# Optimization experiments

Hardware: AMD Instinct MI355X
Metric: run time of the kernel (lower is better)

Reference implementation:

```python
import jax, jax.numpy as jnp
import numpy as np

N = 16384      # number of points
DIM = 128      # feature dim
POS_DIM = 3
K = 16         # neighbors (init kwarg k)
SCALE = np.float32(np.sqrt(DIM))


def setup_inputs() -> dict:
    key = jax.random.key(0)
    ks = jax.random.split(key, 16)
    g = lambda i, shape: (jax.random.normal(ks[i], shape, dtype=jnp.float32) * 0.05)
    return {
        "x": jax.random.normal(ks[0], (N, DIM), dtype=jnp.float32),
        "pos": jax.random.uniform(ks[1], (N, POS_DIM), dtype=jnp.float32),
        # weights stored as (in, out); torch Linear applies x @ W.T + b
        "Wq": g(2, (DIM, DIM)),
        "Wk": g(3, (DIM, DIM)),
        "Wv": g(4, (DIM, DIM)),
        "mid_w1": g(5, (DIM, DIM)), "mid_b1": g(6, (DIM,)),
        "mid_w2": g(7, (DIM, DIM)), "mid_b2": g(8, (DIM,)),
        "pe_w1": g(9, (POS_DIM, DIM)), "pe_b1": g(10, (DIM,)),
        "pe_w2": g(11, (DIM, DIM)), "pe_b2": g(12, (DIM,)),
        "fin_w": g(13, (DIM, DIM)), "fin_b": g(14, (DIM,)),
    }


def _knn_indices(pos):
    # squared pairwise distances [N, N]; top-K smallest -> neighbor indices [N, K]
    sq = jnp.sum(pos * pos, axis=-1)
    d2 = sq[:, None] + sq[None, :] - 2.0 * (pos @ pos.T)
    _, ind = jax.lax.top_k(-d2, K)
    return ind


def reference(x, pos, Wq, Wk, Wv, mid_w1, mid_b1, mid_w2, mid_b2,
              pe_w1, pe_b1, pe_w2, pe_b2, fin_w, fin_b):
    ind = _knn_indices(pos)                    # [N, K] int32 (constant wrt grads)
    x_k = x[ind]                               # [N, K, D]
    pos_k = pos[ind]                           # [N, K, 3]
    rel = pos[:, None, :] - pos_k              # [N, K, 3]
    pe = jax.nn.relu(rel @ pe_w1 + pe_b1) @ pe_w2 + pe_b2    # [N, K, D]
    q = x @ Wq                                 # [N, D]
    h = q[:, None, :] - (x_k @ Wk) + pe        # [N, K, D]
    y = jax.nn.relu(h @ mid_w1 + mid_b1) @ mid_w2 + mid_b2   # [N, K, D]
    y = jax.nn.softmax(y / SCALE, axis=-2)     # softmax over neighbors K
    z = x_k @ Wv + pe                          # [N, K, D]
    agg = jnp.sum(y * z, axis=-2)              # [N, D]
    return agg @ fin_w + fin_b + x
```

## Files before the change

kernel.cpp:

```cpp
#include <hip/hip_runtime.h>
#include <hip/hip_bf16.h>

#define N_PTS 16384
#define DIMF  128
#define KNB   16
#define GRES  8
#define NCELL (GRES*GRES*GRES)

typedef __attribute__((ext_vector_type(8))) short bf16x8;
typedef __attribute__((ext_vector_type(4))) short bf16x4;
typedef __attribute__((ext_vector_type(4))) float f32x4;
typedef __attribute__((ext_vector_type(4))) unsigned int u32x4;
typedef __attribute__((ext_vector_type(2))) unsigned int u32x2;

__device__ __forceinline__ unsigned short f2b(float f){
  unsigned int u = __float_as_uint(f);
  u = u + 0x7fffu + ((u >> 16) & 1u);
  return (unsigned short)(u >> 16);
}
__device__ __forceinline__ unsigned cvtpk(float lo, float hi){
  unsigned r;
  asm("v_cvt_pk_bf16_f32 %0, %1, %2" : "=v"(r) : "v"(lo), "v"(hi));
  return r;
}
__device__ __forceinline__ float b2f(unsigned short u){
  return __uint_as_float(((unsigned)u) << 16);
}
__device__ __forceinline__ float b2fs(short s){
  return __uint_as_float(((unsigned)(unsigned short)s) << 16);
}
__device__ __forceinline__ float unsort_f(unsigned s){
  unsigned u = (s & 0x80000000u) ? (s ^ 0x80000000u) : ~s;
  return __uint_as_float(u);
}

__global__ __launch_bounds__(256) void count_kernel(const float* __restrict__ pos, int* __restrict__ cnt){
  int i = blockIdx.x*256 + threadIdx.x;
  float px = pos[i*3+0], py = pos[i*3+1], pz = pos[i*3+2];
  int cx = min(GRES-1, max(0,(int)(px*(float)GRES)));
  int cy = min(GRES-1, max(0,(int)(py*(float)GRES)));
  int cz = min(GRES-1, max(0,(int)(pz*(float)GRES)));
  atomicAdd(&cnt[(cz*GRES+cy)*GRES+cx], 1);
}

__global__ __launch_bounds__(256) void scan_kernel(const int* __restrict__ cnt, int* __restrict__ starts, int* __restrict__ fillp){
  __shared__ int part[256];
  int t = threadIdx.x;
  int a = cnt[2*t], b = cnt[2*t+1];
  part[t] = a + b;
  __syncthreads();
  if (t == 0){
    int acc = 0;
    for (int i=0;i<256;++i){ int tmp = part[i]; part[i] = acc; acc += tmp; }
  }
  __syncthreads();
  int base = part[t];
  starts[2*t]   = base;     fillp[2*t]   = base;
  starts[2*t+1] = base + a; fillp[2*t+1] = base + a;
}

__global__ __launch_bounds__(256) void scatter_kernel(const float* __restrict__ pos, int* __restrict__ fillp,
                                                      float4* __restrict__ pos4, int* __restrict__ pidx,
                                                      int* __restrict__ inv){
  int i = blockIdx.x*256 + threadIdx.x;
  float px = pos[i*3+0], py = pos[i*3+1], pz = pos[i*3+2];
  int cx = min(GRES-1, max(0,(int)(px*(float)GRES)));
  int cy = min(GRES-1, max(0,(int)(py*(float)GRES)));
  int cz = min(GRES-1, max(0,(int)(pz*(float)GRES)));
  int c = (cz*GRES+cy)*GRES+cx;
  float sq = __fadd_rn(__fadd_rn(__fmul_rn(px,px), __fmul_rn(py,py)), __fmul_rn(pz,pz));
  int s = atomicAdd(&fillp[c], 1);
  pos4[s] = make_float4(px, py, pz, sq);
  pidx[s] = i;
  inv[i] = s;
}

__global__ __launch_bounds__(256) void knn_query64(const float4* __restrict__ pos4, const int* __restrict__ pidx,
                                                   const int* __restrict__ starts, const int* __restrict__ cnt,
                                                   const int* __restrict__ inv,
                                                   int* __restrict__ ind_slot, char* __restrict__ flags){
  __shared__ unsigned long long cand[4][64];
  int lane = threadIdx.x & 63;
  int wv   = threadIdx.x >> 6;
  int t = blockIdx.x*4 + wv;
  float4 qp = pos4[t];
  float qx = qp.x, qy = qp.y, qz = qp.z, qsq = qp.w;
  int cx = min(GRES-1, max(0,(int)(qx*(float)GRES)));
  int cy = min(GRES-1, max(0,(int)(qy*(float)GRES)));
  int cz = min(GRES-1, max(0,(int)(qz*(float)GRES)));
  int zlo = max(0,cz-1), zhi = min(GRES-1,cz+1);
  int ylo = max(0,cy-1), yhi = min(GRES-1,cy+1);
  int xlo = max(0,cx-1), xhi = min(GRES-1,cx+1);

  int nb = 0;
  if (lane < 27){
    int dz = lane/9 - 1, dy = (lane/3)%3 - 1, dx = lane%3 - 1;
    int zz = cz+dz, yy = cy+dy, xx = cx+dx;
    if (zz>=zlo && zz<=zhi && yy>=ylo && yy<=yhi && xx>=xlo && xx<=xhi)
      nb = cnt[(zz*GRES+yy)*GRES+xx];
  }
  #pragma unroll
  for (int o=1;o<64;o<<=1) nb += __shfl_xor(nb, o, 64);
  float V = (float)((zhi-zlo+1)*(yhi-ylo+1)*(xhi-xlo+1)) * 0.001953125f;
  float r3 = 3.8197186f * V / (float)nb;
  float tau2 = 2.0f * __powf(r3, 0.66666667f);

  int nfound = 0;
  bool okscan = false;
  for (int it = 0; it < 8; ++it){
    nfound = 0;
    for (int zz=zlo; zz<=zhi; ++zz)
    for (int yy=ylo; yy<=yhi; ++yy)
    for (int xx=xlo; xx<=xhi; ++xx){
      int c = (zz*GRES+yy)*GRES+xx;
      int s0 = starts[c], n = cnt[c];
      for (int b = 0; b < n; b += 64){
        int o = b + lane;
        bool valid = o < n;
        float d = 3.0e38f; int idx = 0;
        if (valid){
          float4 pc = pos4[s0+o];
          idx = pidx[s0+o];
          float dot = __fmaf_rn(qz, pc.z, __fmaf_rn(qy, pc.y, __fmul_rn(qx, pc.x)));
          d   = __fsub_rn(__fadd_rn(qsq, pc.w), __fmul_rn(2.0f, dot));
        }
        bool admit = valid && (d < tau2);
        unsigned long long mask = __ballot(admit);
        if (admit){
          int pos = nfound + (int)__popcll(mask & ((1ull<<lane)-1ull));
          if (pos < 64){
            unsigned su = __float_as_uint(d);
            su ^= (unsigned)((int)su >> 31) | 0x80000000u;
            cand[wv][pos] = ((unsigned long long)su << 32) | (unsigned)idx;
          }
        }
        nfound += (int)__popcll(mask);
      }
    }
    if (nfound > 64){ tau2 *= 0.7f; continue; }
    if (nfound < 16){ tau2 *= 2.0f; continue; }
    okscan = true; break;
  }
  if (!okscan){ if (lane == 0) flags[t] = 1; return; }

  asm volatile("s_waitcnt lgkmcnt(0)" ::: "memory");
  __builtin_amdgcn_sched_barrier(0);
  unsigned long long key = (lane < nfound) ? cand[wv][lane] : ~0ull;

  #pragma unroll
  for (int k = 2; k <= 64; k <<= 1){
    #pragma unroll
    for (int j = k>>1; j >= 1; j >>= 1){
      unsigned long long other = __shfl_xor(key, j, 64);
      bool takeSmall = (((lane & k) == 0) != ((lane & j) != 0));
      bool less = other < key;
      key = (takeSmall == less) ? other : key;
    }
  }
  if (lane < 16) ind_slot[t*KNB + lane] = inv[(int)(unsigned)(key & 0xffffffffu)];

  unsigned long long k15 = __shfl(key, 15, 64);
  float b16 = unsort_f((unsigned)(k15 >> 32));
  double mg = 1.0e300;
  double dqx=(double)qx, dqy=(double)qy, dqz=(double)qz;
  const double h = 0.125;
  if (cx-1 > 0)      mg = fmin(mg, dqx - (double)(cx-1)*h);
  if (cx+1 < GRES-1) mg = fmin(mg, (double)(cx+2)*h - dqx);
  if (cy-1 > 0)      mg = fmin(mg, dqy - (double)(cy-1)*h);
  if (cy+1 < GRES-1) mg = fmin(mg, (double)(cy+2)*h - dqy);
  if (cz-1 > 0)      mg = fmin(mg, dqz - (double)(cz-1)*h);
  if (cz+1 < GRES-1) mg = fmin(mg, (double)(cz+2)*h - dqz);
  bool ok = (mg*mg > (double)b16 + 1.0e-5);
  if (lane == 0) flags[t] = ok ? 0 : 1;
}

__global__ __launch_bounds__(256) void knn_fallback(const float4* __restrict__ pos4, const int* __restrict__ pidx,
                                                    const int* __restrict__ starts, const int* __restrict__ cnt,
                                                    const int* __restrict__ inv,
                                                    const char* __restrict__ flags, int* __restrict__ ind_slot){
  int t = blockIdx.x*256 + threadIdx.x;
  if (t >= N_PTS || !flags[t]) return;
  float4 qp = pos4[t];
  float qx = qp.x, qy = qp.y, qz = qp.z, qsq = qp.w;
  int cx = min(GRES-1, max(0,(int)(qx*(float)GRES)));
  int cy = min(GRES-1, max(0,(int)(qy*(float)GRES)));
  int cz = min(GRES-1, max(0,(int)(qz*(float)GRES)));
  float bd[KNB]; int bi[KNB];
  #pragma unroll
  for (int k=0;k<KNB;++k){ bd[k] = 3.0e38f; bi[k] = 0x7fffffff; }
  const double cinv = 0.125;
  for (int r = 0; r < GRES; ++r){
    int zlo = max(0, cz-r), zhi = min(GRES-1, cz+r);
    int ylo = max(0, cy-r), yhi = min(GRES-1, cy+r);
    int xlo = max(0, cx-r), xhi = min(GRES-1, cx+r);
    for (int zz = zlo; zz <= zhi; ++zz){
      for (int yy = ylo; yy <= yhi; ++yy){
        for (int xx = xlo; xx <= xhi; ++xx){
          int ring = max(abs(zz-cz), max(abs(yy-cy), abs(xx-cx)));
          if (ring != r) continue;
          int c = (zz*GRES+yy)*GRES+xx;
          int s0 = starts[c], e = s0 + cnt[c];
          for (int s = s0; s < e; ++s){
            float4 pc = pos4[s];
            int idx = pidx[s];
            float dot = __fmaf_rn(qz, pc.z, __fmaf_rn(qy, pc.y, __fmul_rn(qx, pc.x)));
            float d   = __fsub_rn(__fadd_rn(qsq, pc.w), __fmul_rn(2.0f, dot));
            bool adm = (d < bd[KNB-1]) || (d == bd[KNB-1] && idx < bi[KNB-1]);
            if (adm){
              #pragma unroll
              for (int p = KNB-1; p >= 1; --p){
                float pd = bd[p-1]; int pi = bi[p-1];
                bool sh  = (pd > d) || (pd == d && pi > idx);
                bool ins = (!sh) && ((bd[p] > d) || (bd[p] == d && bi[p] > idx));
                bd[p] = sh ? pd : (ins ? d   : bd[p]);
                bi[p] = sh ? pi : (ins ? idx : bi[p]);
              }
              bool s0b = (bd[0] > d) || (bd[0] == d && bi[0] > idx);
              if (s0b){ bd[0] = d; bi[0] = idx; }
            }
          }
        }
      }
    }
    if (bd[KNB-1] < 3.0e37f){
      double mg = 1.0e300;
      double dqx=(double)qx, dqy=(double)qy, dqz=(double)qz;
      if (cx - r > 0)      mg = fmin(mg, dqx - (double)(cx-r)*cinv);
      if (cx + r < GRES-1) mg = fmin(mg, (double)(cx+r+1)*cinv - dqx);
      if (cy - r > 0)      mg = fmin(mg, dqy - (double)(cy-r)*cinv);
      if (cy + r < GRES-1) mg = fmin(mg, (double)(cy+r+1)*cinv - dqy);
      if (cz - r > 0)      mg = fmin(mg, dqz - (double)(cz-r)*cinv);
      if (cz + r < GRES-1) mg = fmin(mg, (double)(cz+r+1)*cinv - dqz);
      if (mg*mg > (double)bd[KNB-1] + 1.0e-5) break;
    }
  }
  #pragma unroll
  for (int k=0;k<KNB;++k) ind_slot[t*KNB + k] = inv[bi[k]];
}

__global__ __launch_bounds__(256) void pack_all(const float* __restrict__ w0, const float* __restrict__ w1,
                                                const float* __restrict__ w2, const float* __restrict__ w3,
                                                const float* __restrict__ w4, const float* __restrict__ w5,
                                                const float* __restrict__ w6,
                                                short* __restrict__ dst){
  int slot = blockIdx.y;
  const float* src = (slot==0)?w0:(slot==1)?w1:(slot==2)?w2:(slot==3)?w3:(slot==4)?w4:(slot==5)?w5:w6;
  int f = blockIdx.x*256 + threadIdx.x;
  int j  = f & 7;
  int ln = (f >> 3) & 63;
  int ks = (f >> 9) & 3;
  int nt = f >> 11;
  int k = ks*32 + ((ln >> 4) << 3) + j;
  int n = nt*16 + (ln & 15);
  dst[slot*16384 + f] = (short)f2b(src[k*DIMF + n]);
}

__global__ __launch_bounds__(256) void proj_kernel(const float* __restrict__ x, const int* __restrict__ pidx,
                                                   const short* __restrict__ pw,
                                                   unsigned short* __restrict__ q, unsigned short* __restrict__ xk,
                                                   unsigned short* __restrict__ xv){
  __shared__ __align__(16) char Abuf[32768];
  int tid = threadIdx.x, lane = tid & 63, wv = tid >> 6;
  int r0 = blockIdx.x * 128;
  {
    int row = tid >> 1, half = tid & 1;
    int orig = pidx[r0 + row];
    const float4* xr = (const float4*)(x + (size_t)orig*DIMF + half*64);
    #pragma unroll
    for (int i=0;i<8;++i){
      float4 a = xr[2*i], b = xr[2*i+1];
      u32x4 u;
      u[0] = cvtpk(a.x, a.y); u[1] = cvtpk(a.z, a.w);
      u[2] = cvtpk(b.x, b.y); u[3] = cvtpk(b.z, b.w);
      *(u32x4*)(&Abuf[row*256 + ((half*128 + i*16) ^ ((row&7)<<4))]) = u;
    }
  }
  __syncthreads();
  #pragma unroll 1
  for (int w = 0; w < 3; ++w){
    const bf16x8* bw = (const bf16x8*)(pw + w*16384);
    unsigned short* dst = (w==0) ? q : (w==1) ? xk : xv;
    f32x4 acc[2][8];
    #pragma unroll
    for (int i=0;i<2;++i)
      #pragma unroll
      for (int nt=0;nt<8;++nt) acc[i][nt] = (f32x4){0.f,0.f,0.f,0.f};
    #pragma unroll
    for (int ks=0;ks<4;++ks){
      int ra = (wv*2)*16 + (lane&15);
      int rb = (wv*2+1)*16 + (lane&15);
      int cb = ks*64 + ((lane>>4)<<4);
      bf16x8 a0 = *(const bf16x8*)(&Abuf[ra*256 + (cb ^ ((ra&7)<<4))]);
      bf16x8 a1 = *(const bf16x8*)(&Abuf[rb*256 + (cb ^ ((rb&7)<<4))]);
      #pragma unroll
      for (int nt=0;nt<8;++nt){
        bf16x8 b = bw[(nt*4+ks)*64 + lane];
        acc[0][nt] = __builtin_amdgcn_mfma_f32_16x16x32_bf16(a0, b, acc[0][nt], 0, 0, 0);
        acc[1][nt] = __builtin_amdgcn_mfma_f32_16x16x32_bf16(a1, b, acc[1][nt], 0, 0, 0);
      }
    }
    #pragma unroll
    for (int i=0;i<2;++i){
      int mt = wv*2+i;
      #pragma unroll
      for (int nt=0;nt<8;++nt){
        int grow = r0 + mt*16 + ((lane>>4)<<2);
        int col = nt*16 + (lane&15);
        unsigned pk01 = cvtpk(acc[i][nt][0], acc[i][nt][1]);
        unsigned pk23 = cvtpk(acc[i][nt][2], acc[i][nt][3]);
        dst[(size_t)(grow+0)*DIMF + col] = (unsigned short)pk01;
        dst[(size_t)(grow+1)*DIMF + col] = (unsigned short)(pk01 >> 16);
        dst[(size_t)(grow+2)*DIMF + col] = (unsigned short)pk23;
        dst[(size_t)(grow+3)*DIMF + col] = (unsigned short)(pk23 >> 16);
      }
    }
  }
}

__global__ __launch_bounds__(512, 2) void main_kernel(
    const float* __restrict__ x, const float4* __restrict__ pos4, const int* __restrict__ pidx,
    const float* __restrict__ pe_w1, const float* __restrict__ pe_b1, const float* __restrict__ pe_b2,
    const float* __restrict__ mid_b1, const float* __restrict__ mid_b2, const float* __restrict__ fin_b,
    const unsigned short* __restrict__ qarr, const unsigned short* __restrict__ xkarr,
    const unsigned short* __restrict__ xvarr,
    const int* __restrict__ ind_slot, const short* __restrict__ pw,
    float* __restrict__ out)
{
  __shared__ __align__(16) char peLDS[32768];
  __shared__ __align__(16) char wbuf[32768];
  __shared__ float aggT[DIMF][8];
  __shared__ int indbuf[128];
  __shared__ int origbuf[8];
  int tid = threadIdx.x;
  int lane = tid & 63;
  int wv = tid >> 6;
  int t0 = blockIdx.x * 8;

  int g = lane >> 4, kl = lane & 15;
  int mt = wv;

  #define STAGE_W(slot) { \
    const char* gsrc = (const char*)(pw + (size_t)(slot)*16384) + wv*4096 + lane*16; \
    char* ldst = &wbuf[wv*4096]; \
    __builtin_amdgcn_global_load_lds(gsrc,        ldst,        16, 0, 0); \
    __builtin_amdgcn_global_load_lds(gsrc + 1024, ldst + 1024, 16, 0, 0); \
    __builtin_amdgcn_global_load_lds(gsrc + 2048, ldst + 2048, 16, 0, 0); \
    __builtin_amdgcn_global_load_lds(gsrc + 3072, ldst + 3072, 16, 0, 0); }

  if (tid < 128) indbuf[tid] = ind_slot[blockIdx.x*128 + tid];
  if (tid < 8) origbuf[tid] = pidx[t0 + tid];
  STAGE_W(3);
  __syncthreads();

  int nb4[4];
  #pragma unroll
  for (int r=0;r<4;++r) nb4[r] = indbuf[mt*16 + g*4 + r];
  int nbr = indbuf[mt*16 + kl];
  unsigned short zraw[8][4];
  #pragma unroll
  for (int nt=0;nt<8;++nt)
    #pragma unroll
    for (int r=0;r<4;++r)
      zraw[nt][r] = xvarr[(size_t)nb4[r]*DIMF + nt*16 + kl];

  bf16x8 tfrag[4];
  {
    float4 pq = pos4[t0+mt];
    float4 pn = pos4[nbr];
    float rx = pq.x-pn.x, ry = pq.y-pn.y, rz = pq.z-pn.z;
    #pragma unroll
    for (int ks=0;ks<4;++ks){
      int c0 = ks*32 + g*8;
      const float4* w0 = (const float4*)(pe_w1 + c0);
      const float4* w1 = (const float4*)(pe_w1 + DIMF + c0);
      const float4* w2 = (const float4*)(pe_w1 + 2*DIMF + c0);
      const float4* bb = (const float4*)(pe_b1 + c0);
      float4 wa0=w0[0], wa1=w0[1], wb0=w1[0], wb1=w1[1], wc0=w2[0], wc1=w2[1], wd0=bb[0], wd1=bb[1];
      float wa[8]={wa0.x,wa0.y,wa0.z,wa0.w,wa1.x,wa1.y,wa1.z,wa1.w};
      float wb[8]={wb0.x,wb0.y,wb0.z,wb0.w,wb1.x,wb1.y,wb1.z,wb1.w};
      float wc[8]={wc0.x,wc0.y,wc0.z,wc0.w,wc1.x,wc1.y,wc1.z,wc1.w};
      float wd[8]={wd0.x,wd0.y,wd0.z,wd0.w,wd1.x,wd1.y,wd1.z,wd1.w};
      float tv[8];
      #pragma unroll
      for (int j=0;j<8;++j)
        tv[j] = fmaxf(fmaf(rx, wa[j], fmaf(ry, wb[j], fmaf(rz, wc[j], wd[j]))), 0.f);
      u32x4 u;
      u[0] = cvtpk(tv[0], tv[1]); u[1] = cvtpk(tv[2], tv[3]);
      u[2] = cvtpk(tv[4], tv[5]); u[3] = cvtpk(tv[6], tv[7]);
      tfrag[ks] = __builtin_bit_cast(bf16x8, u);
    }
  }

  f32x4 acc[8];
  const bf16x8* bw = (const bf16x8*)wbuf;

  {
    #pragma unroll
    for (int nt=0;nt<8;++nt){
      float bv = pe_b2[nt*16 + kl];
      acc[nt] = (f32x4){bv,bv,bv,bv};
    }
    #pragma unroll
    for (int ks=0;ks<4;++ks){
      #pragma unroll
      for (int nt=0;nt<8;++nt){
        bf16x8 b = bw[(nt*4+ks)*64 + lane];
        acc[nt] = __builtin_amdgcn_mfma_f32_16x16x32_bf16(tfrag[ks], b, acc[nt], 0, 0, 0);
      }
    }
  }

  bf16x4 zb[8];
  int r0w = mt*16 + g*4;
  #pragma unroll
  for (int nt=0;nt<8;++nt){
    int col = nt*16 + kl;
    float p0 = acc[nt][0], p1 = acc[nt][1], p2 = acc[nt][2], p3 = acc[nt][3];
    unsigned pk01 = cvtpk(p0, p1), pk23 = cvtpk(p2, p3);
    *(unsigned short*)&peLDS[(r0w+0)*256 + ((col*2) ^ (((r0w+0)&7)<<4))] = (unsigned short)pk01;
    *(unsigned short*)&peLDS[(r0w+1)*256 + ((col*2) ^ (((r0w+1)&7)<<4))] = (unsigned short)(pk01 >> 16);
    *(unsigned short*)&peLDS[(r0w+2)*256 + ((col*2) ^ (((r0w+2)&7)<<4))] = (unsigned short)pk23;
    *(unsigned short*)&peLDS[(r0w+3)*256 + ((col*2) ^ (((r0w+3)&7)<<4))] = (unsigned short)(pk23 >> 16);
    float z0 = b2f(zraw[nt][0]) + p0;
    float z1 = b2f(zraw[nt][1]) + p1;
    float z2 = b2f(zraw[nt][2]) + p2;
    float z3 = b2f(zraw[nt][3]) + p3;
    u32x2 zu; zu[0] = cvtpk(z0, z1); zu[1] = cvtpk(z2, z3);
    zb[nt] = __builtin_bit_cast(bf16x4, zu);
  }

  bf16x8 q8[4], k8[4];
  {
    const unsigned short* qrow = qarr + (size_t)(t0+mt)*DIMF;
    const unsigned short* krow = xkarr + (size_t)nbr*DIMF;
    #pragma unroll
    for (int ks=0;ks<4;++ks){
      int c0 = ks*32 + g*8;
      q8[ks] = *(const bf16x8*)(qrow + c0);
      k8[ks] = *(const bf16x8*)(krow + c0);
    }
  }
  __syncthreads();
  STAGE_W(4);

  bf16x8 hfrag[4];
  {
    int row = mt*16 + kl;
    #pragma unroll
    for (int ks=0;ks<4;++ks){
      int c0 = ks*32 + g*8;
      bf16x8 p8 = *(const bf16x8*)(&peLDS[row*256 + ((c0*2) ^ ((row&7)<<4))]);
      float hf[8];
      #pragma unroll
      for (int j=0;j<8;++j)
        hf[j] = (b2fs(q8[ks][j]) - b2fs(k8[ks][j])) + b2fs(p8[j]);
      u32x4 u;
      u[0] = cvtpk(hf[0], hf[1]); u[1] = cvtpk(hf[2], hf[3]);
      u[2] = cvtpk(hf[4], hf[5]); u[3] = cvtpk(hf[6], hf[7]);
      hfrag[ks] = __builtin_bit_cast(bf16x8, u);
    }
  }
  __syncthreads();

  {
    #pragma unroll
    for (int nt=0;nt<8;++nt){
      float bv = mid_b1[nt*16 + kl];
      acc[nt] = (f32x4){bv,bv,bv,bv};
    }
    #pragma unroll
    for (int ks=0;ks<4;++ks){
      #pragma unroll
      for (int nt=0;nt<8;++nt){
        bf16x8 b = bw[(nt*4+ks)*64 + lane];
        acc[nt] = __builtin_amdgcn_mfma_f32_16x16x32_bf16(hfrag[ks], b, acc[nt], 0, 0, 0);
      }
    }
  }
  __syncthreads();
  STAGE_W(5);
  #pragma unroll
  for (int nt=0;nt<8;++nt){
    int col = nt*16 + kl;
    unsigned pk01 = cvtpk(fmaxf(acc[nt][0],0.f), fmaxf(acc[nt][1],0.f));
    unsigned pk23 = cvtpk(fmaxf(acc[nt][2],0.f), fmaxf(acc[nt][3],0.f));
    *(unsigned short*)&peLDS[(r0w+0)*256 + ((col*2) ^ (((r0w+0)&7)<<4))] = (unsigned short)pk01;
    *(unsigned short*)&peLDS[(r0w+1)*256 + ((col*2) ^ (((r0w+1)&7)<<4))] = (unsigned short)(pk01 >> 16);
    *(unsigned short*)&peLDS[(r0w+2)*256 + ((col*2) ^ (((r0w+2)&7)<<4))] = (unsigned short)pk23;
    *(unsigned short*)&peLDS[(r0w+3)*256 + ((col*2) ^ (((r0w+3)&7)<<4))] = (unsigned short)(pk23 >> 16);
  }
  __syncthreads();

  {
    #pragma unroll
    for (int nt=0;nt<8;++nt){
      float bv = mid_b2[nt*16 + kl];
      acc[nt] = (f32x4){bv,bv,bv,bv};
    }
    #pragma unroll
    for (int ks=0;ks<4;++ks){
      int ra = mt*16 + kl;
      int cb = ks*64 + g*16;
      bf16x8 a0 = *(const bf16x8*)(&peLDS[ra*256 + (cb ^ ((ra&7)<<4))]);
      #pragma unroll
      for (int nt=0;nt<8;++nt){
        bf16x8 b = bw[(nt*4+ks)*64 + lane];
        acc[nt] = __builtin_amdgcn_mfma_f32_16x16x32_bf16(a0, b, acc[nt], 0, 0, 0);
      }
    }
    const float invS = 0.08838834764831843f;
    #pragma unroll
    for (int nt=0;nt<8;++nt){
      f32x4 y = acc[nt];
      float mx = fmaxf(fmaxf(y[0],y[1]), fmaxf(y[2],y[3]));
      mx = fmaxf(mx, __shfl_xor(mx, 16, 64));
      mx = fmaxf(mx, __shfl_xor(mx, 32, 64));
      float e0 = __expf((y[0]-mx)*invS);
      float e1 = __expf((y[1]-mx)*invS);
      float e2 = __expf((y[2]-mx)*invS);
      float e3 = __expf((y[3]-mx)*invS);
      float ssum = e0+e1+e2+e3;
      ssum += __shfl_xor(ssum, 16, 64);
      ssum += __shfl_xor(ssum, 32, 64);
      bf16x4 zv = zb[nt];
      float ps = (e0*b2fs(zv[0]) + e1*b2fs(zv[1]) + e2*b2fs(zv[2]) + e3*b2fs(zv[3])) / ssum;
      ps += __shfl_xor(ps, 16, 64);
      ps += __shfl_xor(ps, 32, 64);
      if (lane < 16) aggT[nt*16 + lane][mt] = ps;
    }
  }
  __syncthreads();
  STAGE_W(6);
  __syncthreads();

  {
    f32x4 facc = (f32x4){0.f,0.f,0.f,0.f};
    #pragma unroll
    for (int ks=0;ks<4;++ks){
      int c0 = ks*32 + g*8;
      float av[8];
      #pragma unroll
      for (int j=0;j<8;++j)
        av[j] = (kl < 8) ? aggT[c0+j][kl] : 0.f;
      u32x4 u;
      u[0] = cvtpk(av[0], av[1]); u[1] = cvtpk(av[2], av[3]);
      u[2] = cvtpk(av[4], av[5]); u[3] = cvtpk(av[6], av[7]);
      bf16x8 a = __builtin_bit_cast(bf16x8, u);
      bf16x8 b = bw[(wv*4+ks)*64 + lane];
      facc = __builtin_amdgcn_mfma_f32_16x16x32_bf16(a, b, facc, 0, 0, 0);
    }
    int col = wv*16 + kl;
    float fb = fin_b[col];
    if (g < 2){
      #pragma unroll
      for (int r=0;r<4;++r){
        int prow = g*4 + r;
        int o = origbuf[prow];
        out[(size_t)o*DIMF + col] = facc[r] + fb + x[(size_t)o*DIMF + col];
      }
    }
  }
  #undef STAGE_W
}

extern "C" void kernel_launch(void* const* d_in, const int* in_sizes, int n_in,
                              void* d_out, int out_size, void* d_ws, size_t ws_size,
                              hipStream_t stream)
{
  (void)in_sizes; (void)n_in; (void)out_size; (void)ws_size;
  const float* x      = (const float*)d_in[0];
  const float* pos    = (const float*)d_in[1];
  const float* Wq     = (const float*)d_in[2];
  const float* Wk     = (const float*)d_in[3];
  const float* Wv     = (const float*)d_in[4];
  const float* mid_w1 = (const float*)d_in[5];
  const float* mid_b1 = (const float*)d_in[6];
  const float* mid_w2 = (const float*)d_in[7];
  const float* mid_b2 = (const float*)d_in[8];
  const float* pe_w1  = (const float*)d_in[9];
  const float* pe_b1  = (const float*)d_in[10];
  const float* pe_w2  = (const float*)d_in[11];
  const float* pe_b2  = (const float*)d_in[12];
  const float* fin_w  = (const float*)d_in[13];
  const float* fin_b  = (const float*)d_in[14];
  float* out = (float*)d_out;
  char* ws = (char*)d_ws;

  int*    cellcnt = (int*)   (ws + 0);
  int*    fillp   = (int*)   (ws + 4096);
  int*    starts  = (int*)   (ws + 8192);
  char*   flags   = (char*)  (ws + 18432);
  int*    pidx    = (int*)   (ws + 49152);
  float4* pos4    = (float4*)(ws + 114688);
  int*    ind     = (int*)   (ws + 376832);
  short*  pw      = (short*) (ws + 1425408);
  int*    inv     = (int*)   (ws + 1654784);
  unsigned short* qarr  = (unsigned short*)(ws + 1720320);
  unsigned short* xkarr = (unsigned short*)(ws + 5914624);
  unsigned short* xvarr = (unsigned short*)(ws + 10108928);

  hipMemsetAsync(cellcnt, 0, NCELL*sizeof(int), stream);
  count_kernel  <<<N_PTS/256, 256, 0, stream>>>(pos, cellcnt);
  scan_kernel   <<<1,         256, 0, stream>>>(cellcnt, starts, fillp);
  scatter_kernel<<<N_PTS/256, 256, 0, stream>>>(pos, fillp, pos4, pidx, inv);
  knn_query64   <<<N_PTS/4,   256, 0, stream>>>(pos4, pidx, starts, cellcnt, inv, ind, flags);
  knn_fallback  <<<N_PTS/256, 256, 0, stream>>>(pos4, pidx, starts, cellcnt, inv, flags, ind);

  pack_all<<<dim3(64,7), 256, 0, stream>>>(Wq, Wk, Wv, pe_w2, mid_w1, mid_w2, fin_w, pw);

  proj_kernel<<<N_PTS/128, 256, 0, stream>>>(x, pidx, pw, qarr, xkarr, xvarr);

  main_kernel<<<N_PTS/8, 512, 0, stream>>>(x, pos4, pidx, pe_w1, pe_b1, pe_b2, mid_b1, mid_b2, fin_b,
                                           qarr, xkarr, xvarr, ind, pw, out);
}
```

Measured before the change: 180.2 us.

## Parallelize cell scan, halve proj tile rows, pad aggT, overlap fin weight staging

Replaces the serial single-thread prefix sum in scan_kernel with a wave shuffle scan plus a cross-wave combine. proj_kernel now processes 64 rows per block instead of 128, which doubles the grid for more parallelism at the cost of reloading weights more often. aggT gets a padding column to reduce LDS bank conflicts. The fin_w staging load is moved before the softmax/aggregation epilogue so it overlaps that compute.

```diff
diff --git a/kernel.cpp b/kernel.cpp
--- a/kernel.cpp
+++ b/kernel.cpp
@@ -44,19 +44,24 @@
 }
 
 __global__ __launch_bounds__(256) void scan_kernel(const int* __restrict__ cnt, int* __restrict__ starts, int* __restrict__ fillp){
-  __shared__ int part[256];
+  __shared__ int wsum[4];
   int t = threadIdx.x;
+  int lane = t & 63, w = t >> 6;
   int a = cnt[2*t], b = cnt[2*t+1];
-  part[t] = a + b;
-  __syncthreads();
-  if (t == 0){
-    int acc = 0;
-    for (int i=0;i<256;++i){ int tmp = part[i]; part[i] = acc; acc += tmp; }
-  }
-  __syncthreads();
-  int base = part[t];
-  starts[2*t]   = base;     fillp[2*t]   = base;
-  starts[2*t+1] = base + a; fillp[2*t+1] = base + a;
+  int s = a + b;
+  int p = s;
+  #pragma unroll
+  for (int off = 1; off < 64; off <<= 1){
+    int v = __shfl_up(p, off, 64);
+    if (lane >= off) p += v;
+  }
+  if (lane == 63) wsum[w] = p;
+  __syncthreads();
+  int base = 0;
+  for (int i = 0; i < w; ++i) base += wsum[i];
+  int excl = base + p - s;
+  starts[2*t]   = excl;     fillp[2*t]   = excl;
+  starts[2*t+1] = excl + a; fillp[2*t+1] = excl + a;
 }
 
 __global__ __launch_bounds__(256) void scatter_kernel(const float* __restrict__ pos, int* __restrict__ fillp,
@@ -259,20 +264,20 @@
                                                    const short* __restrict__ pw,
                                                    unsigned short* __restrict__ q, unsigned short* __restrict__ xk,
                                                    unsigned short* __restrict__ xv){
-  __shared__ __align__(16) char Abuf[32768];
+  __shared__ __align__(16) char Abuf[16384];
   int tid = threadIdx.x, lane = tid & 63, wv = tid >> 6;
-  int r0 = blockIdx.x * 128;
-  {
-    int row = tid >> 1, half = tid & 1;
+  int r0 = blockIdx.x * 64;
+  {
+    int row = tid >> 2, q4 = tid & 3;
     int orig = pidx[r0 + row];
-    const float4* xr = (const float4*)(x + (size_t)orig*DIMF + half*64);
-    #pragma unroll
-    for (int i=0;i<8;++i){
+    const float4* xr = (const float4*)(x + (size_t)orig*DIMF + q4*32);
+    #pragma unroll
+    for (int i=0;i<4;++i){
       float4 a = xr[2*i], b = xr[2*i+1];
       u32x4 u;
       u[0] = cvtpk(a.x, a.y); u[1] = cvtpk(a.z, a.w);
       u[2] = cvtpk(b.x, b.y); u[3] = cvtpk(b.z, b.w);
-      *(u32x4*)(&Abuf[row*256 + ((half*128 + i*16) ^ ((row&7)<<4))]) = u;
+      *(u32x4*)(&Abuf[row*256 + ((q4*64 + i*16) ^ ((row&7)<<4))]) = u;
     }
   }
   __syncthreads();
@@ -280,39 +285,30 @@
   for (int w = 0; w < 3; ++w){
     const bf16x8* bw = (const bf16x8*)(pw + w*16384);
     unsigned short* dst = (w==0) ? q : (w==1) ? xk : xv;
-    f32x4 acc[2][8];
-    #pragma unroll
-    for (int i=0;i<2;++i)
-      #pragma unroll
-      for (int nt=0;nt<8;++nt) acc[i][nt] = (f32x4){0.f,0.f,0.f,0.f};
-    #pragma unroll
-    for (int ks=0;ks<4;++ks){
-      int ra = (wv*2)*16 + (lane&15);
-      int rb = (wv*2+1)*16 + (lane&15);
+    f32x4 acc[8];
+    #pragma unroll
+    for (int nt=0;nt<8;++nt) acc[nt] = (f32x4){0.f,0.f,0.f,0.f};
+    #pragma unroll
+    for (int ks=0;ks<4;++ks){
+      int ra = wv*16 + (lane&15);
       int cb = ks*64 + ((lane>>4)<<4);
       bf16x8 a0 = *(const bf16x8*)(&Abuf[ra*256 + (cb ^ ((ra&7)<<4))]);
-      bf16x8 a1 = *(const bf16x8*)(&Abuf[rb*256 + (cb ^ ((rb&7)<<4))]);
       #pragma unroll
       for (int nt=0;nt<8;++nt){
         bf16x8 b = bw[(nt*4+ks)*64 + lane];
-        acc[0][nt] = __builtin_amdgcn_mfma_f32_16x16x32_bf16(a0, b, acc[0][nt], 0, 0, 0);
-        acc[1][nt] = __builtin_amdgcn_mfma_f32_16x16x32_bf16(a1, b, acc[1][nt], 0, 0, 0);
+        acc[nt] = __builtin_amdgcn_mfma_f32_16x16x32_bf16(a0, b, acc[nt], 0, 0, 0);
       }
     }
     #pragma unroll
-    for (int i=0;i<2;++i){
-      int mt = wv*2+i;
-      #pragma unroll
-      for (int nt=0;nt<8;++nt){
-        int grow = r0 + mt*16 + ((lane>>4)<<2);
-        int col = nt*16 + (lane&15);
-        unsigned pk01 = cvtpk(acc[i][nt][0], acc[i][nt][1]);
-        unsigned pk23 = cvtpk(acc[i][nt][2], acc[i][nt][3]);
-        dst[(size_t)(grow+0)*DIMF + col] = (unsigned short)pk01;
-        dst[(size_t)(grow+1)*DIMF + col] = (unsigned short)(pk01 >> 16);
-        dst[(size_t)(grow+2)*DIMF + col] = (unsigned short)pk23;
-        dst[(size_t)(grow+3)*DIMF + col] = (unsigned short)(pk23 >> 16);
-      }
+    for (int nt=0;nt<8;++nt){
+      int grow = r0 + wv*16 + ((lane>>4)<<2);
+      int col = nt*16 + (lane&15);
+      unsigned pk01 = cvtpk(acc[nt][0], acc[nt][1]);
+      unsigned pk23 = cvtpk(acc[nt][2], acc[nt][3]);
+      dst[(size_t)(grow+0)*DIMF + col] = (unsigned short)pk01;
+      dst[(size_t)(grow+1)*DIMF + col] = (unsigned short)(pk01 >> 16);
+      dst[(size_t)(grow+2)*DIMF + col] = (unsigned short)pk23;
+      dst[(size_t)(grow+3)*DIMF + col] = (unsigned short)(pk23 >> 16);
     }
   }
 }
@@ -328,7 +324,7 @@
 {
   __shared__ __align__(16) char peLDS[32768];
   __shared__ __align__(16) char wbuf[32768];
-  __shared__ float aggT[DIMF][8];
+  __shared__ float aggT[DIMF][9];
   __shared__ int indbuf[128];
   __shared__ int origbuf[8];
   int tid = threadIdx.x;
@@ -508,6 +504,11 @@
         acc[nt] = __builtin_amdgcn_mfma_f32_16x16x32_bf16(a0, b, acc[nt], 0, 0, 0);
       }
     }
+  }
+  __syncthreads();
+  STAGE_W(6);
+
+  {
     const float invS = 0.08838834764831843f;
     #pragma unroll
     for (int nt=0;nt<8;++nt){
@@ -529,8 +530,6 @@
       if (lane < 16) aggT[nt*16 + lane][mt] = ps;
     }
   }
-  __syncthreads();
-  STAGE_W(6);
   __syncthreads();
 
   {
@@ -608,7 +607,7 @@
 
   pack_all<<<dim3(64,7), 256, 0, stream>>>(Wq, Wk, Wv, pe_w2, mid_w1, mid_w2, fin_w, pw);
 
-  proj_kernel<<<N_PTS/128, 256, 0, stream>>>(x, pidx, pw, qarr, xkarr, xvarr);
+  proj_kernel<<<N_PTS/64, 256, 0, stream>>>(x, pidx, pw, qarr, xkarr, xvarr);
 
   main_kernel<<<N_PTS/8, 512, 0, stream>>>(x, pos4, pidx, pe_w1, pe_b1, pe_b2, mid_b1, mid_b2, fin_b,
                                            qarr, xkarr, xvarr, ind, pw, out);
```

Measured after the change: 164.9 us. 8.5% less time.
